# Optimization experiments

Hardware: AMD Instinct MI355X
Metric: run time of the kernel (lower is better)

Reference implementation:

```python
import jax, jax.numpy as jnp
import numpy as np

B = 32          # batch size
N = 32          # image dim -> P = N*N points per sample
P = N * N
F = 64          # point feature dim (= MLP output)
K = 32          # max_neighbors
R = 0.1         # ball-query radius
EPS = 1e-5      # batchnorm eps


def setup_inputs() -> dict:
    key = jax.random.key(0)
    ks = jax.random.split(key, 4)
    NP = B * P
    x = jax.random.normal(ks[0], (NP, F), jnp.float32)
    pos = jax.random.uniform(ks[1], (NP, 2), jnp.float32)
    # module requires exactly N*N points per sample, sorted by batch
    batch = jnp.repeat(jnp.arange(B, dtype=jnp.int32), P)
    # MLP([66,128,64]) params: Linear->BN->ReLU->Linear
    W1 = jax.random.normal(ks[2], (F + 2, 128), jnp.float32) * (1.0 / np.sqrt(F + 2))
    b1 = jnp.zeros((128,), jnp.float32)
    gamma1 = jnp.ones((128,), jnp.float32)
    beta1 = jnp.zeros((128,), jnp.float32)
    W2 = jax.random.normal(ks[3], (128, F), jnp.float32) * (1.0 / np.sqrt(128))
    b2 = jnp.zeros((F,), jnp.float32)
    return {"x": x, "pos": pos, "batch": batch, "W1": W1, "b1": b1,
            "gamma1": gamma1, "beta1": beta1, "W2": W2, "b2": b2}


def reference(x, pos, batch, W1, b1, gamma1, beta1, W2, b2):
    NP = x.shape[0]
    posb = pos.reshape(B, P, 2)
    # pixel (target) index of every query point: batch*N*N + row*N + col
    rows = jnp.clip((pos[:, 1] * N).astype(jnp.int32), 0, N - 1)
    cols = jnp.clip((pos[:, 0] * N).astype(jnp.int32), 0, N - 1)
    pix = batch.astype(jnp.int32) * (N * N) + rows * N + cols          # [NP]
    # radius ball query within each batch sample (deterministic: nearest-K within R)
    d2 = jnp.sum((posb[:, :, None, :] - posb[:, None, :, :]) ** 2, -1)  # [B,P,P]
    d2 = jnp.where(d2 <= R * R, d2, jnp.inf)
    negd, nbr = jax.lax.top_k(-d2, K)                                   # [B,P,K]
    valid = jnp.isfinite(negd)
    src = (jnp.arange(B, dtype=jnp.int32)[:, None, None] * P + nbr).reshape(-1)  # [B*P*K]
    dst = jnp.broadcast_to(pix.reshape(B, P)[:, :, None], (B, P, K)).reshape(-1)
    mask = valid.reshape(-1) & (src != dst)          # remove_self_loops
    # PointNetConv message: concat(x_j, pos_j - pos_i); pos_i indexed by mapped target
    relpos = pos[src] - pos[dst]
    msg_nb = jnp.concatenate([x[src], relpos], -1)                    # [B*P*K, F+2]
    # add_self_loops: edge (i, i) for every node -> relpos = 0
    msg_self = jnp.concatenate([x, jnp.zeros_like(pos)], -1)          # [NP, F+2]
    msg = jnp.concatenate([msg_nb, msg_self], 0)
    m = jnp.concatenate([mask, jnp.ones((NP,), bool)], 0)
    tgt = jnp.concatenate([dst, jnp.arange(NP, dtype=jnp.int32)], 0)
    # MLP: Linear -> BatchNorm(training stats over valid messages) -> ReLU -> Linear
    z = msg @ W1 + b1
    mf = m.astype(z.dtype)[:, None]
    cnt = jnp.sum(mf)
    mean = jnp.sum(z * mf, 0, keepdims=True) / cnt
    var = jnp.sum(((z - mean) ** 2) * mf, 0, keepdims=True) / cnt
    h = jax.nn.relu((z - mean) / jnp.sqrt(var + EPS) * gamma1 + beta1)
    o = h @ W2 + b2                                                    # [M, F]
    # scatter-max aggregation into B*N*N pixel nodes (self loops make all nonempty)
    o = jnp.where(m[:, None], o, -jnp.inf)
    pixel_features = jax.ops.segment_max(o, tgt, num_segments=NP)
    images = pixel_features.reshape(B, N, N, F).transpose(0, 3, 1, 2)
    return images
```

## Files before the change

kernel.cpp:

```cpp
#include <hip/hip_runtime.h>
#include <hip/hip_bf16.h>
#include <hip/hip_fp16.h>
#include <math.h>


#define NPTS   32768
#define KNB    32
#define BN_EPS 1e-5f

#define WS_NBRS     0u
#define WS_NBRCNT   4194304u
#define WS_SCSH     4719616u
#define WS_W2B      4720640u
#define WS_PART     4737024u
#define WS_Y        5265408u
#define WS_SCRATCH  5265408u
#define WS_WB       13654016u
#define WS_QCNT     22042624u
#define WS_QSTART   22173696u
#define WS_QLIST    22304768u
#define WS_ISLOT    22435840u
#define WS_SELF     22566912u
#define WS_SHP      30955520u
#define WS_BQPART   22566912u

typedef __attribute__((ext_vector_type(8))) _Float16 half8;
typedef __attribute__((ext_vector_type(2))) _Float16 half2v;
typedef __attribute__((ext_vector_type(4))) float floatx4;

__device__ __forceinline__ unsigned short f2h_bits(float f) {
    _Float16 h = (_Float16)f;
    return *reinterpret_cast<unsigned short*>(&h);
}
__device__ __forceinline__ float bf_lo(unsigned int w) { return __uint_as_float(w << 16); }
__device__ __forceinline__ float bf_hi(unsigned int w) { return __uint_as_float(w & 0xffff0000u); }
__device__ __forceinline__ unsigned int pack_bf2(float lo, float hi) {
    __hip_bfloat162 hh = __float22bfloat162_rn(make_float2(lo, hi));
    return *reinterpret_cast<unsigned int*>(&hh);
}
__device__ __forceinline__ unsigned int pack_h2(float lo, float hi) {
    half2v hh = { (_Float16)lo, (_Float16)hi };
    return *reinterpret_cast<unsigned int*>(&hh);
}

union ShBQ {
    struct {
        float2 poss[1024];
        float accd[1024], accx[1024], accy[1024];
        unsigned long long cand[4][256];
    } bq;
    struct {
        int cntS[1024], preS[1024], offS[1024], pixOf[1024];
        int wtot[4];
    } pm;
};

__launch_bounds__(256)
__global__ void k_bq(const float* __restrict__ pos,
                     int* __restrict__ nbrs, int* __restrict__ nbr_cnt,
                     float* __restrict__ bqpart,
                     const float* __restrict__ W2, unsigned short* __restrict__ w2b,
                     int* __restrict__ qcnt, int* __restrict__ qstart,
                     int* __restrict__ qlist, int* __restrict__ islot) {
    __shared__ ShBQ sh;
    int tid = threadIdx.x;

    if (blockIdx.x < 32) {
        int s = blockIdx.x;
        int gt = s * 256 + tid;
        {
            int j  = gt & 7;
            int L  = (gt >> 3) & 63;
            int ks = (gt >> 9) & 3;
            int t4 = gt >> 11;
            int k = ks * 32 + (L >> 4) * 8 + j;
            int n = t4 * 16 + (L & 15);
            w2b[gt] = f2h_bits(W2[k * 64 + n]);
        }
        int base = s << 10;
        for (int i = tid; i < 1024; i += 256) sh.pm.cntS[i] = 0;
        __syncthreads();
        for (int ql = tid; ql < 1024; ql += 256) {
            float2 p = *(const float2*)&pos[2 * (base + ql)];
            int row = min(max((int)(p.y * 32.0f), 0), 31);
            int col = min(max((int)(p.x * 32.0f), 0), 31);
            int pixl = row * 32 + col;
            sh.pm.pixOf[ql] = pixl;
            atomicAdd(&sh.pm.cntS[pixl], 1);
        }
        __syncthreads();
        int a0 = sh.pm.cntS[4 * tid], a1 = sh.pm.cntS[4 * tid + 1];
        int a2 = sh.pm.cntS[4 * tid + 2], a3 = sh.pm.cntS[4 * tid + 3];
        int tsum = a0 + a1 + a2 + a3;
        int lane = tid & 63, wv = tid >> 6;
        int v = tsum;
        for (int o = 1; o < 64; o <<= 1) { int u = __shfl_up(v, o); if (lane >= o) v += u; }
        if (lane == 63) sh.pm.wtot[wv] = v;
        __syncthreads();
        int wbase = 0;
        for (int w = 0; w < wv; ++w) wbase += sh.pm.wtot[w];
        int excl = wbase + v - tsum;
        sh.pm.preS[4 * tid] = excl;
        sh.pm.preS[4 * tid + 1] = excl + a0;
        sh.pm.preS[4 * tid + 2] = excl + a0 + a1;
        sh.pm.preS[4 * tid + 3] = excl + a0 + a1 + a2;
        __syncthreads();
        for (int i = tid; i < 1024; i += 256) sh.pm.offS[i] = sh.pm.preS[i];
        __syncthreads();
        for (int ql = tid; ql < 1024; ql += 256) {
            int p = sh.pm.pixOf[ql];
            int slot = atomicAdd(&sh.pm.offS[p], 1);
            qlist[base + slot] = base + ql;
            islot[base + ql] = base + slot;
        }
        for (int i = tid; i < 1024; i += 256) {
            qcnt[base + i] = sh.pm.cntS[i];
            qstart[base + i] = base + sh.pm.preS[i];
        }
        return;
    }

    int bqphys = blockIdx.x - 32;
    int bqid = (bqphys & 7) * 128 + (bqphys >> 3);
    int wave = tid >> 6, lane = tid & 63;
    int s = bqid >> 5;
    int chunk = bqid & 31;
    int base = s << 10;
    for (int i = tid; i < 1024; i += 256) sh.bq.poss[i] = *(const float2*)&pos[2 * (base + i)];
    for (int i = tid; i < 1024; i += 256) { sh.bq.accd[i] = 0.0f; sh.bq.accx[i] = 0.0f; sh.bq.accy[i] = 0.0f; }
    __syncthreads();
    float2 pr[16];
#pragma unroll
    for (int k = 0; k < 16; ++k) pr[k] = sh.bq.poss[k * 64 + lane];
    unsigned long long lb = (1ull << lane) - 1ull;

    float aD = 0, aE = 0, aF = 0;
    for (int qi = 0; qi < 8; ++qi) {
        int ql = chunk * 32 + wave * 8 + qi;
        int q = base + ql;
        float2 qp = sh.bq.poss[ql];
        int row = min(max((int)(qp.y * 32.0f), 0), 31);
        int col = min(max((int)(qp.x * 32.0f), 0), 31);
        int pixl = row * 32 + col;
        float2 tp = sh.bq.poss[pixl];
        int cnt = 0;
        __builtin_amdgcn_wave_barrier();
#pragma unroll
        for (int k = 0; k < 16; ++k) {
            float dx = pr[k].x - qp.x, dy = pr[k].y - qp.y;
            float d2 = __fadd_rn(__fmul_rn(dx, dx), __fmul_rn(dy, dy));
            bool pred = (d2 <= 0.01f);
            unsigned long long mask = __ballot(pred);
            if (pred) {
                int slot = cnt + (int)__popcll(mask & lb);
                if (slot < 256)
                    sh.bq.cand[wave][slot] = ((unsigned long long)__float_as_uint(d2) << 32)
                                             | (unsigned int)(k * 64 + lane);
            }
            cnt += (int)__popcll(mask);
        }
        cnt = min(cnt, 256);
        __builtin_amdgcn_wave_barrier();
        int osel = 0;
        for (int cb = 0; cb < cnt; cb += 64) {
            int i = cb + lane;
            bool sel = false;
            int j = 0;
            if (i < cnt) {
                unsigned long long key = sh.bq.cand[wave][i];
                j = (int)(key & 0xffffffffu);
                if (cnt <= KNB) {
                    sel = (j != pixl);
                } else {
                    int rank = 0;
                    for (int t = 0; t < cnt; ++t) rank += (sh.bq.cand[wave][t] < key) ? 1 : 0;
                    sel = (rank < KNB) && (j != pixl);
                }
            }
            unsigned long long mask = __ballot(sel);
            if (sel) {
                int slot = osel + (int)__popcll(mask & lb);
                nbrs[q * KNB + slot] = base + j;
                float rx = sh.bq.poss[j].x - tp.x, ry = sh.bq.poss[j].y - tp.y;
                aD += rx * rx; aE += rx * ry; aF += ry * ry;
                atomicAdd(&sh.bq.accd[j], 1.0f);
                atomicAdd(&sh.bq.accx[j], tp.x);
                atomicAdd(&sh.bq.accy[j], tp.y);
            }
            osel += (int)__popcll(mask);
        }
        if (lane >= osel && lane < KNB) nbrs[q * KNB + lane] = base;
        if (lane == 0) nbr_cnt[q] = osel;
    }
#pragma unroll
    for (int o = 1; o < 64; o <<= 1) {
        aD += __shfl_xor(aD, o); aE += __shfl_xor(aE, o); aF += __shfl_xor(aF, o);
    }
    __syncthreads();
    float* pb = &bqpart[bqid * 3076];
    for (int i = tid; i < 1024; i += 256) {
        pb[i] = sh.bq.accd[i]; pb[1024 + i] = sh.bq.accx[i]; pb[2048 + i] = sh.bq.accy[i];
    }
    if (tid == 0) { pb[3072] = aD; pb[3073] = aE; pb[3074] = aF; }
}

__launch_bounds__(512)
__global__ void k_y(const float* __restrict__ x, const float* __restrict__ W1,
                    const float* __restrict__ b1, const float* __restrict__ pos,
                    const float* __restrict__ bqpart,
                    unsigned int* __restrict__ yb, float* __restrict__ partials) {
    __shared__ float w1s[64 * 128];
    __shared__ float stage[8][512];
    __shared__ float lsum[515];
    __shared__ float degS[128], stxS[128], styS[128];
    int tid = threadIdx.x;
    int vb = (blockIdx.x & 7) * 32 + (blockIdx.x >> 3);
    int nblock = vb * 128;
    for (int i = tid; i < 64 * 128; i += 512) w1s[i] = W1[i];
    for (int i = tid; i < 515; i += 512) lsum[i] = 0.0f;
    if (tid < 128) {
        int n = nblock + tid;
        int s = n >> 10, off = n & 1023;
        const float* pb = &bqpart[(s * 32) * 3076];
        float d = 0, xx = 0, yy = 0;
        for (int j = 0; j < 32; ++j) {
            d  += pb[j * 3076 + off];
            xx += pb[j * 3076 + 1024 + off];
            yy += pb[j * 3076 + 2048 + off];
        }
        degS[tid] = d; stxS[tid] = xx; styS[tid] = yy;
    }
    __syncthreads();
    int wave = tid >> 6, lane = tid & 63;
    int f0 = 2 * lane, f1 = 2 * lane + 1;
    float b10 = b1[f0], b11 = b1[f1];
    float* st = &stage[wave][0];
    float P0 = 0, Q0 = 0, R0 = 0, S0 = 0, P1 = 0, Q1 = 0, R1 = 0, S1 = 0;
    float sB = 0, sC = 0, sDeg = 0;

    for (int it = 0; it < 2; ++it) {
        int nbase = nblock + (wave * 2 + it) * 8;
        __builtin_amdgcn_wave_barrier();
#pragma unroll
        for (int mm = 0; mm < 8; ++mm)
            st[mm * 64 + lane] = x[(nbase + mm) * 64 + lane];
        __builtin_amdgcn_wave_barrier();
        float z0[8], z1[8];
#pragma unroll
        for (int mm = 0; mm < 8; ++mm) { z0[mm] = b10; z1[mm] = b11; }
        for (int k4 = 0; k4 < 16; ++k4) {
            float2 wv0 = *(const float2*)&w1s[(k4 * 4 + 0) * 128 + f0];
            float2 wv1 = *(const float2*)&w1s[(k4 * 4 + 1) * 128 + f0];
            float2 wv2 = *(const float2*)&w1s[(k4 * 4 + 2) * 128 + f0];
            float2 wv3 = *(const float2*)&w1s[(k4 * 4 + 3) * 128 + f0];
#pragma unroll
            for (int mm = 0; mm < 8; ++mm) {
                float4 mk = *(const float4*)&st[mm * 64 + k4 * 4];
                z0[mm] += mk.x * wv0.x + mk.y * wv1.x + mk.z * wv2.x + mk.w * wv3.x;
                z1[mm] += mk.x * wv0.y + mk.y * wv1.y + mk.z * wv2.y + mk.w * wv3.y;
            }
        }
#pragma unroll
        for (int mm = 0; mm < 8; ++mm) {
            int n = nbase + mm;
            int li = n - nblock;
            float dg = degS[li];
            float wgt = 1.0f + dg;
            float Bn = dg * pos[2 * n]     - stxS[li];
            float Cn = dg * pos[2 * n + 1] - styS[li];
            float a = z0[mm], bq = z1[mm];
            P0 += wgt * a;  Q0 += wgt * a * a;  R0 += a * Bn;  S0 += a * Cn;
            P1 += wgt * bq; Q1 += wgt * bq * bq; R1 += bq * Bn; S1 += bq * Cn;
            sB += Bn; sC += Cn; sDeg += dg;
            yb[n * 64 + lane] = pack_bf2(a, bq);
        }
        __builtin_amdgcn_wave_barrier();
    }
    atomicAdd(&lsum[f0], P0);        atomicAdd(&lsum[f1], P1);
    atomicAdd(&lsum[128 + f0], Q0);  atomicAdd(&lsum[128 + f1], Q1);
    atomicAdd(&lsum[256 + f0], R0);  atomicAdd(&lsum[256 + f1], R1);
    atomicAdd(&lsum[384 + f0], S0);  atomicAdd(&lsum[384 + f1], S1);
    if (lane == 0) {
        atomicAdd(&lsum[512], sB);
        atomicAdd(&lsum[513], sC);
        atomicAdd(&lsum[514], sDeg);
    }
    __syncthreads();
    for (int i = tid; i < 515; i += 512) partials[blockIdx.x * 516 + i] = lsum[i];
}

__global__ void k_finalize(const float* __restrict__ gamma, const float* __restrict__ beta,
                           const float* __restrict__ W1, const float* __restrict__ partials,
                           const float* __restrict__ bqpart, float* __restrict__ scsh) {
    __shared__ float red[515];
    __shared__ float sDEF[3];
    int tid = threadIdx.x;
    if (tid < 3) sDEF[tid] = 0.0f;
    for (int i = tid; i < 515; i += 256) {
        float s = 0;
        for (int b = 0; b < 256; ++b) s += partials[b * 516 + i];
        red[i] = s;
    }
    __syncthreads();
    {
        float td = 0, te = 0, tf = 0;
        for (int b = tid; b < 1024; b += 256) {
            const float* pb = &bqpart[b * 3076 + 3072];
            td += pb[0]; te += pb[1]; tf += pb[2];
        }
        atomicAdd(&sDEF[0], td); atomicAdd(&sDEF[1], te); atomicAdd(&sDEF[2], tf);
    }
    __syncthreads();
    if (tid < 128) {
        int f = tid;
        float P = red[f], Q = red[128 + f], R = red[256 + f], S = red[384 + f];
        float SB = red[512], SC = red[513], SDeg = red[514];
        float u = W1[8192 + f], v = W1[8320 + f];
        float cntv = 32768.0f + SDeg;
        float mean = (P + u * SB + v * SC) / cntv;
        float E2 = (Q + 2.0f * u * R + 2.0f * v * S
                    + u * u * sDEF[0] + 2.0f * u * v * sDEF[1] + v * v * sDEF[2]) / cntv;
        float var = E2 - mean * mean;
        float sc = gamma[f] / sqrtf(var + BN_EPS);
        scsh[f] = sc;
        scsh[128 + f] = beta[f] - mean * sc;
    }
}

__launch_bounds__(256)
__global__ void k_self(const unsigned int* __restrict__ yb, const float* __restrict__ pos,
                       const float* __restrict__ W1, const float* __restrict__ scsh,
                       const unsigned short* __restrict__ w2b, const float* __restrict__ b2,
                       const int* __restrict__ qcnt,
                       unsigned int* __restrict__ wbuf, unsigned int* __restrict__ shpbuf,
                       float* __restrict__ selfbuf, float* __restrict__ out) {
    __shared__ unsigned short hbuf[4][16 * 136];
    int tid = threadIdx.x, wave = tid >> 6, lane = tid & 63;
    unsigned short* hb = hbuf[wave];
    half8 bfrag[4][4];
#pragma unroll
    for (int t = 0; t < 4; ++t)
#pragma unroll
        for (int ks = 0; ks < 4; ++ks)
            bfrag[t][ks] = *(const half8*)&w2b[((t * 4 + ks) * 64 + lane) * 8];
    int f0 = 2 * lane;
    float sc0 = scsh[f0],     sh0 = scsh[128 + f0];
    float sc1 = scsh[f0 + 1], sh1 = scsh[129 + f0];
    float u0 = W1[8192 + f0], v0 = W1[8320 + f0];
    float u1 = W1[8193 + f0], v1 = W1[8321 + f0];
    float b2v0 = b2[(lane & 15)],      b2v1 = b2[16 + (lane & 15)];
    float b2v2 = b2[32 + (lane & 15)], b2v3 = b2[48 + (lane & 15)];

    int vb = (blockIdx.x & 7) * 64 + (blockIdx.x >> 3);
    int nbase = (vb * 4 + wave) * 16;
#pragma unroll
    for (int c = 0; c < 2; ++c) {
        unsigned int yw[8];
#pragma unroll
        for (int j = 0; j < 8; ++j)
            yw[j] = yb[(nbase + c * 8 + j) * 64 + lane];
#pragma unroll
        for (int j = 0; j < 8; ++j) {
            int e = c * 8 + j;
            int nn = nbase + e;
            float y0 = bf_lo(yw[j]), y1 = bf_hi(yw[j]);
            float h0 = fmaxf(y0 * sc0 + sh0, 0.0f);
            float h1 = fmaxf(y1 * sc1 + sh1, 0.0f);
            *(unsigned int*)&hb[e * 136 + f0] = pack_h2(h0, h1);
            float px = pos[2 * nn], py = pos[2 * nn + 1];
            float ts0 = (px * u0 + py * v0) * sc0;
            float ts1 = (px * u1 + py * v1) * sc1;
            wbuf[nn * 64 + lane]   = pack_h2(y0 * sc0 + ts0, y1 * sc1 + ts1);
            shpbuf[nn * 64 + lane] = pack_h2(sh0 - ts0, sh1 - ts1);
        }
    }
    __builtin_amdgcn_wave_barrier();
    floatx4 acc0 = {0,0,0,0}, acc1 = {0,0,0,0}, acc2 = {0,0,0,0}, acc3 = {0,0,0,0};
#pragma unroll
    for (int ks = 0; ks < 4; ++ks) {
        half8 a = *(const half8*)&hb[(lane & 15) * 136 + ks * 32 + (lane >> 4) * 8];
        acc0 = __builtin_amdgcn_mfma_f32_16x16x32_f16(a, bfrag[0][ks], acc0, 0, 0, 0);
        acc1 = __builtin_amdgcn_mfma_f32_16x16x32_f16(a, bfrag[1][ks], acc1, 0, 0, 0);
        acc2 = __builtin_amdgcn_mfma_f32_16x16x32_f16(a, bfrag[2][ks], acc2, 0, 0, 0);
        acc3 = __builtin_amdgcn_mfma_f32_16x16x32_f16(a, bfrag[3][ks], acc3, 0, 0, 0);
    }
    int nrow = nbase + (lane >> 4) * 4;
#pragma unroll
    for (int r = 0; r < 4; ++r) {
        int n = nrow + r;
        float o0 = acc0[r] + b2v0, o1 = acc1[r] + b2v1;
        float o2 = acc2[r] + b2v2, o3 = acc3[r] + b2v3;
        selfbuf[n * 64 + (lane & 15)]      = o0;
        selfbuf[n * 64 + 16 + (lane & 15)] = o1;
        selfbuf[n * 64 + 32 + (lane & 15)] = o2;
        selfbuf[n * 64 + 48 + (lane & 15)] = o3;
        if (qcnt[n] == 0) {
            int obase = (n >> 10) * 65536 + (n & 1023);
            out[obase + ((lane & 15)) * 1024]      = o0;
            out[obase + (16 + (lane & 15)) * 1024] = o1;
            out[obase + (32 + (lane & 15)) * 1024] = o2;
            out[obase + (48 + (lane & 15)) * 1024] = o3;
        }
    }
}

__launch_bounds__(256)
__global__ void k_out(const unsigned int* __restrict__ wbuf,
                      const unsigned int* __restrict__ shpbuf,
                      const float* __restrict__ pos,
                      const unsigned short* __restrict__ w2b, const float* __restrict__ b2,
                      const int* __restrict__ nbrs, const int* __restrict__ nbr_cnt,
                      const int* __restrict__ islot, float* __restrict__ scratch) {
    int tid = threadIdx.x, wave = tid >> 6, lane = tid & 63;
    half8 bfrag[4][4];
#pragma unroll
    for (int t = 0; t < 4; ++t)
#pragma unroll
        for (int ks = 0; ks < 4; ++ks)
            bfrag[t][ks] = *(const half8*)&w2b[((t * 4 + ks) * 64 + lane) * 8];
    float b2l = b2[lane];
    int em = lane & 15;
    int koff = (lane >> 4) * 4;
    int vb = (blockIdx.x & 7) * 512 + (blockIdx.x >> 3);
    int wid = vb * 4 + wave;
    int q0 = wid * 2, q1 = q0 + 1;

    int m0 = nbr_cnt[q0], m1 = nbr_cnt[q1];
    int nv0 = nbrs[q0 * KNB + (lane & 31)];
    int nv1 = nbrs[q1 * KNB + (lane & 31)];
    float2 qp0 = *(const float2*)&pos[2 * q0];
    float2 qp1 = *(const float2*)&pos[2 * q1];
    int is0 = islot[q0], is1 = islot[q1];

    int row0 = min(max((int)(qp0.y * 32.0f), 0), 31);
    int col0 = min(max((int)(qp0.x * 32.0f), 0), 31);
    int pixq0 = ((q0 >> 10) << 10) + row0 * 32 + col0;
    int row1 = min(max((int)(qp1.y * 32.0f), 0), 31);
    int col1 = min(max((int)(qp1.x * 32.0f), 0), 31);
    int pixq1 = ((q1 >> 10) << 10) + row1 * 32 + col1;

    uint4 sv0[4], sv1[4];
#pragma unroll
    for (int ks = 0; ks < 4; ++ks) {
        sv0[ks] = *(const uint4*)&shpbuf[pixq0 * 64 + ks * 16 + koff];
        sv1[ks] = *(const uint4*)&shpbuf[pixq1 * 64 + ks * 16 + koff];
    }

#pragma unroll
    for (int qi = 0; qi < 2; ++qi) {
        int m   = qi ? m1 : m0;
        int nv  = qi ? nv1 : nv0;
        int isq = qi ? is1 : is0;
        float om0[4], om1[4], om2[4], om3[4];
#pragma unroll
        for (int r = 0; r < 4; ++r) { om0[r] = -INFINITY; om1[r] = -INFINITY; om2[r] = -INFINITY; om3[r] = -INFINITY; }

        int src0 = __shfl(nv, em);
        int src1 = __shfl(nv, 16 + em);
        uint4 g0[4], g1[4];
        const unsigned int* wp0 = &wbuf[src0 * 64 + koff];
        const unsigned int* wp1 = &wbuf[src1 * 64 + koff];
#pragma unroll
        for (int ks = 0; ks < 4; ++ks) g0[ks] = *(const uint4*)&wp0[ks * 16];
#pragma unroll
        for (int ks = 0; ks < 4; ++ks) g1[ks] = *(const uint4*)&wp1[ks * 16];

        int rowb = (lane >> 4) * 4;
        {
            floatx4 a0 = {0,0,0,0}, a1 = {0,0,0,0}, a2 = {0,0,0,0}, a3 = {0,0,0,0};
#pragma unroll
            for (int ks = 0; ks < 4; ++ks) {
                union { unsigned int u[4]; half8 h8; } af;
                uint4 gg = g0[ks];
                uint4 ss = qi ? sv1[ks] : sv0[ks];
#pragma unroll
                for (int qd = 0; qd < 4; ++qd) {
                    unsigned int wd = (qd == 0) ? gg.x : (qd == 1) ? gg.y : (qd == 2) ? gg.z : gg.w;
                    unsigned int sd = (qd == 0) ? ss.x : (qd == 1) ? ss.y : (qd == 2) ? ss.z : ss.w;
                    half2v wh = *reinterpret_cast<half2v*>(&wd);
                    half2v shh = *reinterpret_cast<half2v*>(&sd);
                    half2v zz = { (_Float16)0.0f, (_Float16)0.0f };
                    half2v hh = __builtin_elementwise_max(wh + shh, zz);
                    af.u[qd] = *reinterpret_cast<unsigned int*>(&hh);
                }
                a0 = __builtin_amdgcn_mfma_f32_16x16x32_f16(af.h8, bfrag[0][ks], a0, 0, 0, 0);
                a1 = __builtin_amdgcn_mfma_f32_16x16x32_f16(af.h8, bfrag[1][ks], a1, 0, 0, 0);
                a2 = __builtin_amdgcn_mfma_f32_16x16x32_f16(af.h8, bfrag[2][ks], a2, 0, 0, 0);
                a3 = __builtin_amdgcn_mfma_f32_16x16x32_f16(af.h8, bfrag[3][ks], a3, 0, 0, 0);
            }
#pragma unroll
            for (int r = 0; r < 4; ++r) {
                if (rowb + r < m) {
                    om0[r] = fmaxf(om0[r], a0[r]);
                    om1[r] = fmaxf(om1[r], a1[r]);
                    om2[r] = fmaxf(om2[r], a2[r]);
                    om3[r] = fmaxf(om3[r], a3[r]);
                }
            }
        }
        {
            floatx4 a0 = {0,0,0,0}, a1 = {0,0,0,0}, a2 = {0,0,0,0}, a3 = {0,0,0,0};
#pragma unroll
            for (int ks = 0; ks < 4; ++ks) {
                union { unsigned int u[4]; half8 h8; } af;
                uint4 gg = g1[ks];
                uint4 ss = qi ? sv1[ks] : sv0[ks];
#pragma unroll
                for (int qd = 0; qd < 4; ++qd) {
                    unsigned int wd = (qd == 0) ? gg.x : (qd == 1) ? gg.y : (qd == 2) ? gg.z : gg.w;
                    unsigned int sd = (qd == 0) ? ss.x : (qd == 1) ? ss.y : (qd == 2) ? ss.z : ss.w;
                    half2v wh = *reinterpret_cast<half2v*>(&wd);
                    half2v shh = *reinterpret_cast<half2v*>(&sd);
                    half2v zz = { (_Float16)0.0f, (_Float16)0.0f };
                    half2v hh = __builtin_elementwise_max(wh + shh, zz);
                    af.u[qd] = *reinterpret_cast<unsigned int*>(&hh);
                }
                a0 = __builtin_amdgcn_mfma_f32_16x16x32_f16(af.h8, bfrag[0][ks], a0, 0, 0, 0);
                a1 = __builtin_amdgcn_mfma_f32_16x16x32_f16(af.h8, bfrag[1][ks], a1, 0, 0, 0);
                a2 = __builtin_amdgcn_mfma_f32_16x16x32_f16(af.h8, bfrag[2][ks], a2, 0, 0, 0);
                a3 = __builtin_amdgcn_mfma_f32_16x16x32_f16(af.h8, bfrag[3][ks], a3, 0, 0, 0);
            }
#pragma unroll
            for (int r = 0; r < 4; ++r) {
                int e = 16 + rowb + r;
                if (e < m) {
                    om0[r] = fmaxf(om0[r], a0[r]);
                    om1[r] = fmaxf(om1[r], a1[r]);
                    om2[r] = fmaxf(om2[r], a2[r]);
                    om3[r] = fmaxf(om3[r], a3[r]);
                }
            }
        }
        float w0 = fmaxf(fmaxf(om0[0], om0[1]), fmaxf(om0[2], om0[3]));
        float w1 = fmaxf(fmaxf(om1[0], om1[1]), fmaxf(om1[2], om1[3]));
        float w2 = fmaxf(fmaxf(om2[0], om2[1]), fmaxf(om2[2], om2[3]));
        float w3 = fmaxf(fmaxf(om3[0], om3[1]), fmaxf(om3[2], om3[3]));
        w0 = fmaxf(w0, __shfl_xor(w0, 16)); w0 = fmaxf(w0, __shfl_xor(w0, 32));
        w1 = fmaxf(w1, __shfl_xor(w1, 16)); w1 = fmaxf(w1, __shfl_xor(w1, 32));
        w2 = fmaxf(w2, __shfl_xor(w2, 16)); w2 = fmaxf(w2, __shfl_xor(w2, 32));
        w3 = fmaxf(w3, __shfl_xor(w3, 16)); w3 = fmaxf(w3, __shfl_xor(w3, 32));
        int g4 = lane >> 4;
        float vf = (g4 == 0) ? w0 : (g4 == 1) ? w1 : (g4 == 2) ? w2 : w3;
        vf += b2l;
        scratch[isq * 64 + lane] = vf;
    }
}

__launch_bounds__(256)
__global__ void k_gather(const float* __restrict__ scratch, const float* __restrict__ selfbuf,
                         const int* __restrict__ qcnt, const int* __restrict__ qstart,
                         float* __restrict__ out) {
    int tid = threadIdx.x, wave = tid >> 6, lane = tid & 63;
    int vb = (blockIdx.x & 7) * 1024 + (blockIdx.x >> 3);
    int n = vb * 4 + wave;
    int c = qcnt[n];
    if (c == 0) return;
    int qs = qstart[n];
    float v = selfbuf[n * 64 + lane];
    for (int i = 0; i < c; ++i)
        v = fmaxf(v, scratch[(qs + i) * 64 + lane]);
    out[(n >> 10) * 65536 + lane * 1024 + (n & 1023)] = v;
}

extern "C" void kernel_launch(void* const* d_in, const int* in_sizes, int n_in,
                              void* d_out, int out_size, void* d_ws, size_t ws_size,
                              hipStream_t stream) {
    const float* x     = (const float*)d_in[0];
    const float* pos   = (const float*)d_in[1];
    const float* W1    = (const float*)d_in[3];
    const float* b1    = (const float*)d_in[4];
    const float* gamma = (const float*)d_in[5];
    const float* beta  = (const float*)d_in[6];
    const float* W2    = (const float*)d_in[7];
    const float* b2    = (const float*)d_in[8];
    float* out = (float*)d_out;
    char* ws = (char*)d_ws;
    int*   nbrs     = (int*)(ws + WS_NBRS);
    int*   nbr_cnt  = (int*)(ws + WS_NBRCNT);
    float* scsh     = (float*)(ws + WS_SCSH);
    unsigned short* w2b = (unsigned short*)(ws + WS_W2B);
    float* partials = (float*)(ws + WS_PART);
    unsigned int* yb = (unsigned int*)(ws + WS_Y);
    float* scratch  = (float*)(ws + WS_SCRATCH);
    unsigned int* wbuf = (unsigned int*)(ws + WS_WB);
    int* qcnt   = (int*)(ws + WS_QCNT);
    int* qstart = (int*)(ws + WS_QSTART);
    int* qlist  = (int*)(ws + WS_QLIST);
    int* islot  = (int*)(ws + WS_ISLOT);
    float* selfbuf = (float*)(ws + WS_SELF);
    unsigned int* shpbuf = (unsigned int*)(ws + WS_SHP);
    float* bqpart   = (float*)(ws + WS_BQPART);

    k_bq<<<1056, 256, 0, stream>>>(pos, nbrs, nbr_cnt, bqpart, W2, w2b,
                                   qcnt, qstart, qlist, islot);
    k_y<<<256, 512, 0, stream>>>(x, W1, b1, pos, bqpart, yb, partials);
    k_finalize<<<1, 256, 0, stream>>>(gamma, beta, W1, partials, bqpart, scsh);
    k_self<<<NPTS / 64, 256, 0, stream>>>(yb, pos, W1, scsh, w2b, b2, qcnt,
                                          wbuf, shpbuf, selfbuf, out);
    k_out<<<NPTS / 8, 256, 0, stream>>>(wbuf, shpbuf, pos, w2b, b2,
                                        nbrs, nbr_cnt, islot, scratch);
    k_gather<<<NPTS / 4, 256, 0, stream>>>(scratch, selfbuf, qcnt, qstart, out);
}
```

Baseline: 243.7 us.

## Switch k_out to 32x32x16 MFMA with one query per wave

Rewrites the neighbor-message output kernel to use 32x32x16 f16 MFMAs, so each wave handles all 32 neighbors of a single query in one tile. Previously it used 16x16x32 MFMAs over two 16-neighbor halves and two queries per wave. A second W2 fragment layout matching the 32x32 operand format is precomputed in k_bq, the grid doubles, and s_setprio is raised around the MFMA loop. The aim is fewer MFMA and shuffle instructions and simpler masking, at the cost of holding more registers in flight per wave and fewer queries per wave.

```diff
diff --git a/kernel.cpp b/kernel.cpp
--- a/kernel.cpp
+++ b/kernel.cpp
@@ -10,6 +10,7 @@
 
 #define WS_NBRS     0u
 #define WS_NBRCNT   4194304u
+#define WS_W2B32    4325376u
 #define WS_SCSH     4719616u
 #define WS_W2B      4720640u
 #define WS_PART     4737024u
@@ -27,6 +28,7 @@
 typedef __attribute__((ext_vector_type(8))) _Float16 half8;
 typedef __attribute__((ext_vector_type(2))) _Float16 half2v;
 typedef __attribute__((ext_vector_type(4))) float floatx4;
+typedef __attribute__((ext_vector_type(16))) float floatx16;
 
 __device__ __forceinline__ unsigned short f2h_bits(float f) {
     _Float16 h = (_Float16)f;
@@ -60,6 +62,7 @@
                      int* __restrict__ nbrs, int* __restrict__ nbr_cnt,
                      float* __restrict__ bqpart,
                      const float* __restrict__ W2, unsigned short* __restrict__ w2b,
+                     unsigned short* __restrict__ w2b32,
                      int* __restrict__ qcnt, int* __restrict__ qstart,
                      int* __restrict__ qlist, int* __restrict__ islot) {
     __shared__ ShBQ sh;
@@ -76,6 +79,15 @@
             int k = ks * 32 + (L >> 4) * 8 + j;
             int n = t4 * 16 + (L & 15);
             w2b[gt] = f2h_bits(W2[k * 64 + n]);
+        }
+        {
+            int j  = gt & 7;
+            int L  = (gt >> 3) & 63;
+            int p  = gt >> 9;
+            int ks = p >> 1, nh = p & 1;
+            int k = ks * 16 + (L >> 5) * 8 + j;
+            int n = nh * 32 + (L & 31);
+            w2b32[gt] = f2h_bits(W2[k * 64 + n]);
         }
         int base = s << 10;
         for (int i = tid; i < 1024; i += 256) sh.pm.cntS[i] = 0;
@@ -408,142 +420,73 @@
 __global__ void k_out(const unsigned int* __restrict__ wbuf,
                       const unsigned int* __restrict__ shpbuf,
                       const float* __restrict__ pos,
-                      const unsigned short* __restrict__ w2b, const float* __restrict__ b2,
+                      const unsigned short* __restrict__ w2b32, const float* __restrict__ b2,
                       const int* __restrict__ nbrs, const int* __restrict__ nbr_cnt,
                       const int* __restrict__ islot, float* __restrict__ scratch) {
     int tid = threadIdx.x, wave = tid >> 6, lane = tid & 63;
-    half8 bfrag[4][4];
-#pragma unroll
-    for (int t = 0; t < 4; ++t)
-#pragma unroll
-        for (int ks = 0; ks < 4; ++ks)
-            bfrag[t][ks] = *(const half8*)&w2b[((t * 4 + ks) * 64 + lane) * 8];
+    half8 bfrag[8][2];
+#pragma unroll
+    for (int ks = 0; ks < 8; ++ks)
+#pragma unroll
+        for (int nh = 0; nh < 2; ++nh)
+            bfrag[ks][nh] = *(const half8*)&w2b32[((ks * 2 + nh) * 64 + lane) * 8];
     float b2l = b2[lane];
-    int em = lane & 15;
-    int koff = (lane >> 4) * 4;
-    int vb = (blockIdx.x & 7) * 512 + (blockIdx.x >> 3);
-    int wid = vb * 4 + wave;
-    int q0 = wid * 2, q1 = q0 + 1;
-
-    int m0 = nbr_cnt[q0], m1 = nbr_cnt[q1];
-    int nv0 = nbrs[q0 * KNB + (lane & 31)];
-    int nv1 = nbrs[q1 * KNB + (lane & 31)];
-    float2 qp0 = *(const float2*)&pos[2 * q0];
-    float2 qp1 = *(const float2*)&pos[2 * q1];
-    int is0 = islot[q0], is1 = islot[q1];
-
-    int row0 = min(max((int)(qp0.y * 32.0f), 0), 31);
-    int col0 = min(max((int)(qp0.x * 32.0f), 0), 31);
-    int pixq0 = ((q0 >> 10) << 10) + row0 * 32 + col0;
-    int row1 = min(max((int)(qp1.y * 32.0f), 0), 31);
-    int col1 = min(max((int)(qp1.x * 32.0f), 0), 31);
-    int pixq1 = ((q1 >> 10) << 10) + row1 * 32 + col1;
-
-    uint4 sv0[4], sv1[4];
-#pragma unroll
-    for (int ks = 0; ks < 4; ++ks) {
-        sv0[ks] = *(const uint4*)&shpbuf[pixq0 * 64 + ks * 16 + koff];
-        sv1[ks] = *(const uint4*)&shpbuf[pixq1 * 64 + ks * 16 + koff];
-    }
-
-#pragma unroll
-    for (int qi = 0; qi < 2; ++qi) {
-        int m   = qi ? m1 : m0;
-        int nv  = qi ? nv1 : nv0;
-        int isq = qi ? is1 : is0;
-        float om0[4], om1[4], om2[4], om3[4];
-#pragma unroll
-        for (int r = 0; r < 4; ++r) { om0[r] = -INFINITY; om1[r] = -INFINITY; om2[r] = -INFINITY; om3[r] = -INFINITY; }
-
-        int src0 = __shfl(nv, em);
-        int src1 = __shfl(nv, 16 + em);
-        uint4 g0[4], g1[4];
-        const unsigned int* wp0 = &wbuf[src0 * 64 + koff];
-        const unsigned int* wp1 = &wbuf[src1 * 64 + koff];
-#pragma unroll
-        for (int ks = 0; ks < 4; ++ks) g0[ks] = *(const uint4*)&wp0[ks * 16];
-#pragma unroll
-        for (int ks = 0; ks < 4; ++ks) g1[ks] = *(const uint4*)&wp1[ks * 16];
-
-        int rowb = (lane >> 4) * 4;
-        {
-            floatx4 a0 = {0,0,0,0}, a1 = {0,0,0,0}, a2 = {0,0,0,0}, a3 = {0,0,0,0};
-#pragma unroll
-            for (int ks = 0; ks < 4; ++ks) {
-                union { unsigned int u[4]; half8 h8; } af;
-                uint4 gg = g0[ks];
-                uint4 ss = qi ? sv1[ks] : sv0[ks];
-#pragma unroll
-                for (int qd = 0; qd < 4; ++qd) {
-                    unsigned int wd = (qd == 0) ? gg.x : (qd == 1) ? gg.y : (qd == 2) ? gg.z : gg.w;
-                    unsigned int sd = (qd == 0) ? ss.x : (qd == 1) ? ss.y : (qd == 2) ? ss.z : ss.w;
-                    half2v wh = *reinterpret_cast<half2v*>(&wd);
-                    half2v shh = *reinterpret_cast<half2v*>(&sd);
-                    half2v zz = { (_Float16)0.0f, (_Float16)0.0f };
-                    half2v hh = __builtin_elementwise_max(wh + shh, zz);
-                    af.u[qd] = *reinterpret_cast<unsigned int*>(&hh);
-                }
-                a0 = __builtin_amdgcn_mfma_f32_16x16x32_f16(af.h8, bfrag[0][ks], a0, 0, 0, 0);
-                a1 = __builtin_amdgcn_mfma_f32_16x16x32_f16(af.h8, bfrag[1][ks], a1, 0, 0, 0);
-                a2 = __builtin_amdgcn_mfma_f32_16x16x32_f16(af.h8, bfrag[2][ks], a2, 0, 0, 0);
-                a3 = __builtin_amdgcn_mfma_f32_16x16x32_f16(af.h8, bfrag[3][ks], a3, 0, 0, 0);
-            }
-#pragma unroll
-            for (int r = 0; r < 4; ++r) {
-                if (rowb + r < m) {
-                    om0[r] = fmaxf(om0[r], a0[r]);
-                    om1[r] = fmaxf(om1[r], a1[r]);
-                    om2[r] = fmaxf(om2[r], a2[r]);
-                    om3[r] = fmaxf(om3[r], a3[r]);
-                }
-            }
-        }
-        {
-            floatx4 a0 = {0,0,0,0}, a1 = {0,0,0,0}, a2 = {0,0,0,0}, a3 = {0,0,0,0};
-#pragma unroll
-            for (int ks = 0; ks < 4; ++ks) {
-                union { unsigned int u[4]; half8 h8; } af;
-                uint4 gg = g1[ks];
-                uint4 ss = qi ? sv1[ks] : sv0[ks];
-#pragma unroll
-                for (int qd = 0; qd < 4; ++qd) {
-                    unsigned int wd = (qd == 0) ? gg.x : (qd == 1) ? gg.y : (qd == 2) ? gg.z : gg.w;
-                    unsigned int sd = (qd == 0) ? ss.x : (qd == 1) ? ss.y : (qd == 2) ? ss.z : ss.w;
-                    half2v wh = *reinterpret_cast<half2v*>(&wd);
-                    half2v shh = *reinterpret_cast<half2v*>(&sd);
-                    half2v zz = { (_Float16)0.0f, (_Float16)0.0f };
-                    half2v hh = __builtin_elementwise_max(wh + shh, zz);
-                    af.u[qd] = *reinterpret_cast<unsigned int*>(&hh);
-                }
-                a0 = __builtin_amdgcn_mfma_f32_16x16x32_f16(af.h8, bfrag[0][ks], a0, 0, 0, 0);
-                a1 = __builtin_amdgcn_mfma_f32_16x16x32_f16(af.h8, bfrag[1][ks], a1, 0, 0, 0);
-                a2 = __builtin_amdgcn_mfma_f32_16x16x32_f16(af.h8, bfrag[2][ks], a2, 0, 0, 0);
-                a3 = __builtin_amdgcn_mfma_f32_16x16x32_f16(af.h8, bfrag[3][ks], a3, 0, 0, 0);
-            }
-#pragma unroll
-            for (int r = 0; r < 4; ++r) {
-                int e = 16 + rowb + r;
-                if (e < m) {
-                    om0[r] = fmaxf(om0[r], a0[r]);
-                    om1[r] = fmaxf(om1[r], a1[r]);
-                    om2[r] = fmaxf(om2[r], a2[r]);
-                    om3[r] = fmaxf(om3[r], a3[r]);
-                }
-            }
-        }
-        float w0 = fmaxf(fmaxf(om0[0], om0[1]), fmaxf(om0[2], om0[3]));
-        float w1 = fmaxf(fmaxf(om1[0], om1[1]), fmaxf(om1[2], om1[3]));
-        float w2 = fmaxf(fmaxf(om2[0], om2[1]), fmaxf(om2[2], om2[3]));
-        float w3 = fmaxf(fmaxf(om3[0], om3[1]), fmaxf(om3[2], om3[3]));
-        w0 = fmaxf(w0, __shfl_xor(w0, 16)); w0 = fmaxf(w0, __shfl_xor(w0, 32));
-        w1 = fmaxf(w1, __shfl_xor(w1, 16)); w1 = fmaxf(w1, __shfl_xor(w1, 32));
-        w2 = fmaxf(w2, __shfl_xor(w2, 16)); w2 = fmaxf(w2, __shfl_xor(w2, 32));
-        w3 = fmaxf(w3, __shfl_xor(w3, 16)); w3 = fmaxf(w3, __shfl_xor(w3, 32));
-        int g4 = lane >> 4;
-        float vf = (g4 == 0) ? w0 : (g4 == 1) ? w1 : (g4 == 2) ? w2 : w3;
-        vf += b2l;
-        scratch[isq * 64 + lane] = vf;
-    }
+    int kc = (lane >> 5) * 4;
+    int vb = (blockIdx.x & 7) * 1024 + (blockIdx.x >> 3);
+    int q = vb * 4 + wave;
+
+    int m = nbr_cnt[q];
+    int isq = islot[q];
+    int nv = nbrs[q * KNB + (lane & 31)];
+    float2 qp = *(const float2*)&pos[2 * q];
+
+    const unsigned int* wp = &wbuf[nv * 64 + kc];
+    uint4 g[8];
+#pragma unroll
+    for (int ks = 0; ks < 8; ++ks) g[ks] = *(const uint4*)&wp[ks * 8];
+
+    int row = min(max((int)(qp.y * 32.0f), 0), 31);
+    int col = min(max((int)(qp.x * 32.0f), 0), 31);
+    int pixq = ((q >> 10) << 10) + row * 32 + col;
+    const unsigned int* sp = &shpbuf[pixq * 64 + kc];
+    uint4 sv[8];
+#pragma unroll
+    for (int ks = 0; ks < 8; ++ks) sv[ks] = *(const uint4*)&sp[ks * 8];
+
+    floatx16 acc0 = {}, acc1 = {};
+    __builtin_amdgcn_s_setprio(1);
+#pragma unroll
+    for (int ks = 0; ks < 8; ++ks) {
+        union { unsigned int u[4]; half8 h8; } af;
+        uint4 gg = g[ks], ss = sv[ks];
+#pragma unroll
+        for (int qd = 0; qd < 4; ++qd) {
+            unsigned int wd = (qd == 0) ? gg.x : (qd == 1) ? gg.y : (qd == 2) ? gg.z : gg.w;
+            unsigned int sd = (qd == 0) ? ss.x : (qd == 1) ? ss.y : (qd == 2) ? ss.z : ss.w;
+            half2v wh = *reinterpret_cast<half2v*>(&wd);
+            half2v shh = *reinterpret_cast<half2v*>(&sd);
+            half2v zz = { (_Float16)0.0f, (_Float16)0.0f };
+            half2v hh = __builtin_elementwise_max(wh + shh, zz);
+            af.u[qd] = *reinterpret_cast<unsigned int*>(&hh);
+        }
+        acc0 = __builtin_amdgcn_mfma_f32_32x32x16_f16(af.h8, bfrag[ks][0], acc0, 0, 0, 0);
+        acc1 = __builtin_amdgcn_mfma_f32_32x32x16_f16(af.h8, bfrag[ks][1], acc1, 0, 0, 0);
+    }
+    __builtin_amdgcn_s_setprio(0);
+
+    int rbase = 4 * (lane >> 5);
+    float v0 = -INFINITY, v1 = -INFINITY;
+#pragma unroll
+    for (int i = 0; i < 16; ++i) {
+        int r = (i & 3) + 8 * (i >> 2) + rbase;
+        bool ok = r < m;
+        v0 = fmaxf(v0, ok ? acc0[i] : -INFINITY);
+        v1 = fmaxf(v1, ok ? acc1[i] : -INFINITY);
+    }
+    v0 = fmaxf(v0, __shfl_xor(v0, 32));
+    v1 = fmaxf(v1, __shfl_xor(v1, 32));
+    float vf = ((lane < 32) ? v0 : v1) + b2l;
+    scratch[isq * 64 + lane] = vf;
 }
 
 __launch_bounds__(256)
@@ -579,6 +522,7 @@
     int*   nbr_cnt  = (int*)(ws + WS_NBRCNT);
     float* scsh     = (float*)(ws + WS_SCSH);
     unsigned short* w2b = (unsigned short*)(ws + WS_W2B);
+    unsigned short* w2b32 = (unsigned short*)(ws + WS_W2B32);
     float* partials = (float*)(ws + WS_PART);
     unsigned int* yb = (unsigned int*)(ws + WS_Y);
     float* scratch  = (float*)(ws + WS_SCRATCH);
@@ -591,13 +535,13 @@
     unsigned int* shpbuf = (unsigned int*)(ws + WS_SHP);
     float* bqpart   = (float*)(ws + WS_BQPART);
 
-    k_bq<<<1056, 256, 0, stream>>>(pos, nbrs, nbr_cnt, bqpart, W2, w2b,
+    k_bq<<<1056, 256, 0, stream>>>(pos, nbrs, nbr_cnt, bqpart, W2, w2b, w2b32,
                                    qcnt, qstart, qlist, islot);
     k_y<<<256, 512, 0, stream>>>(x, W1, b1, pos, bqpart, yb, partials);
     k_finalize<<<1, 256, 0, stream>>>(gamma, beta, W1, partials, bqpart, scsh);
     k_self<<<NPTS / 64, 256, 0, stream>>>(yb, pos, W1, scsh, w2b, b2, qcnt,
                                           wbuf, shpbuf, selfbuf, out);
-    k_out<<<NPTS / 8, 256, 0, stream>>>(wbuf, shpbuf, pos, w2b, b2,
+    k_out<<<NPTS / 4, 256, 0, stream>>>(wbuf, shpbuf, pos, w2b32, b2,
                                         nbrs, nbr_cnt, islot, scratch);
     k_gather<<<NPTS / 4, 256, 0, stream>>>(scratch, selfbuf, qcnt, qstart, out);
 }
```

New measurement: 249.2 us. 1.02x slower.
